# Kernel tuning notes

Measured on AMD Instinct MI355X. Metric: run time of the kernel, lower is better.

## Reference

```python
import jax, jax.numpy as jnp
import numpy as np

D_MODEL = 1024
NUM_HEADS = 16
D_K = D_MODEL // NUM_HEADS


def setup_inputs() -> dict:
    key = jax.random.key(0)
    ks = jax.random.split(key, 11)
    B, S = 2, 2048
    scale = 1.0 / np.sqrt(D_MODEL)
    inp = {
        "query": jax.random.normal(ks[0], (B, S, D_MODEL), jnp.float32),
        "key": jax.random.normal(ks[1], (B, S, D_MODEL), jnp.float32),
        "value": jax.random.normal(ks[2], (B, S, D_MODEL), jnp.float32),
        "Wq": jax.random.normal(ks[3], (D_MODEL, D_MODEL), jnp.float32) * scale,
        "bq": jnp.zeros((D_MODEL,), jnp.float32),
        "Wk": jax.random.normal(ks[4], (D_MODEL, D_MODEL), jnp.float32) * scale,
        "bk": jnp.zeros((D_MODEL,), jnp.float32),
        "Wv": jax.random.normal(ks[5], (D_MODEL, D_MODEL), jnp.float32) * scale,
        "bv": jnp.zeros((D_MODEL,), jnp.float32),
        "Wo": jax.random.normal(ks[6], (D_MODEL, D_MODEL), jnp.float32) * scale,
        "bo": jnp.zeros((D_MODEL,), jnp.float32),
    }
    return inp


def _split_heads(x):
    B, S, _ = x.shape
    return x.reshape(B, S, NUM_HEADS, D_K).transpose(0, 2, 1, 3)  # [B,H,S,d_k]


def reference(query, key, value, Wq, bq, Wk, bk, Wv, bv, Wo, bo):
    # Linear projections (torch Linear: x @ W.T + b)
    q = _split_heads(query @ Wq.T + bq)
    k = _split_heads(key @ Wk.T + bk)
    v = _split_heads(value @ Wv.T + bv)
    scores = jnp.einsum("bhqd,bhkd->bhqk", q, k) / jnp.sqrt(jnp.float32(D_K))
    probs = jax.nn.softmax(scores, axis=-1)
    out = jnp.einsum("bhqk,bhkd->bhqd", probs, v)  # [B,H,S,d_k]
    B, H, S, _ = out.shape
    out = out.transpose(0, 2, 1, 3).reshape(B, S, D_MODEL)
    return out @ Wo.T + bo
```

## Files before the change

kernel.cpp:

```cpp
#include <hip/hip_runtime.h>

#define D_MODEL 1024
#define NHEADS  16
#define DK      64
#define SEQ     2048
#define NBATCH  2
#define MTOT    (NBATCH * SEQ)

typedef _Float16 f16;
typedef _Float16 f16x4 __attribute__((ext_vector_type(4)));
typedef _Float16 f16x8 __attribute__((ext_vector_type(8)));
typedef float    f32x4 __attribute__((ext_vector_type(4)));
typedef float    f32x16 __attribute__((ext_vector_type(16)));

#define LOG2E 1.44269504088896340736f

__global__ __launch_bounds__(256) void cvt_f32_to_f16(
    const float* __restrict__ q, const float* __restrict__ k, const float* __restrict__ v,
    const float* __restrict__ wq, const float* __restrict__ wk,
    const float* __restrict__ wv, const float* __restrict__ wo,
    f16* __restrict__ qf, f16* __restrict__ kf, f16* __restrict__ vf,
    f16* __restrict__ wqh, f16* __restrict__ wkh, f16* __restrict__ wvh, f16* __restrict__ woh)
{
    const int z = blockIdx.y;
    const float* src; f16* dst; int n4;
    if (z == 0)      { src = q;  dst = qf;  n4 = MTOT * D_MODEL / 4; }
    else if (z == 1) { src = k;  dst = kf;  n4 = MTOT * D_MODEL / 4; }
    else if (z == 2) { src = v;  dst = vf;  n4 = MTOT * D_MODEL / 4; }
    else if (z == 3) { src = wq; dst = wqh; n4 = D_MODEL * D_MODEL / 4; }
    else if (z == 4) { src = wk; dst = wkh; n4 = D_MODEL * D_MODEL / 4; }
    else if (z == 5) { src = wv; dst = wvh; n4 = D_MODEL * D_MODEL / 4; }
    else             { src = wo; dst = woh; n4 = D_MODEL * D_MODEL / 4; }
    for (int i = blockIdx.x * 256 + threadIdx.x; i < n4; i += gridDim.x * 256) {
        float4 t = ((const float4*)src)[i];
        f16x4 o = {(f16)t.x, (f16)t.y, (f16)t.z, (f16)t.w};
        ((f16x4*)dst)[i] = o;
    }
}

__device__ __forceinline__ void gemm128_core(
    const f16* __restrict__ A, const f16* __restrict__ Wm,
    int m0, int n0, int kbeg, int kend, f32x16 (&acc)[2][2])
{
    __shared__ __align__(16) f16 As[4096];
    __shared__ __align__(16) f16 Bs[4096];

    const int t    = threadIdx.x;
    const int lane = t & 63;
    const int w    = t >> 6;
    const int l31  = lane & 31, kg = lane >> 5;
    const int wr   = w >> 1,    wc = w & 1;

    size_t offA[2], offB[2];
#pragma unroll
    for (int jj = 0; jj < 2; ++jj) {
        int s  = (w * 2 + jj) * 64 + lane;
        int ko = s >> 7, m = s & 127;
        offA[jj] = (size_t)(m0 + m) * D_MODEL + ko * 8;
        offB[jj] = (size_t)(n0 + m) * D_MODEL + ko * 8;
    }
    const int jb = __builtin_amdgcn_readfirstlane(w * 1024);

#pragma unroll
    for (int i = 0; i < 2; ++i)
#pragma unroll
        for (int j = 0; j < 2; ++j)
#pragma unroll
            for (int r = 0; r < 16; ++r) acc[i][j][r] = 0.f;

    auto* ldsA = (__attribute__((address_space(3))) f16*)As;
    auto* ldsB = (__attribute__((address_space(3))) f16*)Bs;

    for (int k0 = kbeg; k0 < kend; k0 += 32) {
#pragma unroll
        for (int jj = 0; jj < 2; ++jj) {
            __builtin_amdgcn_global_load_lds(
                (const __attribute__((address_space(1))) void*)(A + offA[jj] + k0),
                (__attribute__((address_space(3))) void*)(ldsA + jb + jj * 512),
                16, 0, 0);
            __builtin_amdgcn_global_load_lds(
                (const __attribute__((address_space(1))) void*)(Wm + offB[jj] + k0),
                (__attribute__((address_space(3))) void*)(ldsB + jb + jj * 512),
                16, 0, 0);
        }
        __syncthreads();

#pragma unroll
        for (int step = 0; step < 2; ++step) {
            const int ko = kg + 2 * step;
            f16x8 aF[2], bF[2];
#pragma unroll
            for (int ti = 0; ti < 2; ++ti) {
                aF[ti] = *(const f16x8*)&As[(ko * 128 + wr * 64 + ti * 32 + l31) * 8];
                bF[ti] = *(const f16x8*)&Bs[(ko * 128 + wc * 64 + ti * 32 + l31) * 8];
            }
#pragma unroll
            for (int ti = 0; ti < 2; ++ti)
#pragma unroll
                for (int tj = 0; tj < 2; ++tj)
                    acc[ti][tj] = __builtin_amdgcn_mfma_f32_32x32x16_f16(
                        aF[ti], bF[tj], acc[ti][tj], 0, 0, 0);
        }
        __syncthreads();
    }
}

__global__ __launch_bounds__(256, 3) void qkv_gemm(
    const f16* __restrict__ Qf, const f16* __restrict__ Kf, const f16* __restrict__ Vf,
    const f16* __restrict__ Wqh, const f16* __restrict__ Wkh, const f16* __restrict__ Wvh,
    const float* __restrict__ bq, const float* __restrict__ bk, const float* __restrict__ bv,
    f16* __restrict__ Qh, f16* __restrict__ Kh, f16* __restrict__ Vt)
{
    const int z = blockIdx.z;
    const f16*   A    = z == 0 ? Qf  : z == 1 ? Kf  : Vf;
    const f16*   Wm   = z == 0 ? Wqh : z == 1 ? Wkh : Wvh;
    const float* bias = z == 0 ? bq  : z == 1 ? bk  : bv;

    const int m0 = blockIdx.y * 128, n0 = blockIdx.x * 128;
    f32x16 acc[2][2];
    gemm128_core(A, Wm, m0, n0, 0, D_MODEL, acc);

    const int t = threadIdx.x, lane = t & 63, w = t >> 6;
    const int l31 = lane & 31, kg = lane >> 5;
    const int wr = w >> 1, wc = w & 1;

    if (z < 2) {
        f16* Out = z == 0 ? Qh : Kh;
        const float sc = z == 0 ? 0.125f * LOG2E : 1.0f;
#pragma unroll
        for (int tj = 0; tj < 2; ++tj) {
            const int col = n0 + wc * 64 + tj * 32 + l31;
            const float bc = bias[col];
#pragma unroll
            for (int ti = 0; ti < 2; ++ti)
#pragma unroll
                for (int r = 0; r < 16; ++r) {
                    const int row = m0 + wr * 64 + ti * 32 + (r & 3) + 8 * (r >> 2) + 4 * kg;
                    Out[(size_t)row * D_MODEL + col] = (f16)((acc[ti][tj][r] + bc) * sc);
                }
        }
    } else {
#pragma unroll
        for (int tj = 0; tj < 2; ++tj) {
            const int col = n0 + wc * 64 + tj * 32 + l31;
            const float bc = bias[col];
            const int h = col >> 6, d = col & 63;
#pragma unroll
            for (int ti = 0; ti < 2; ++ti)
#pragma unroll
                for (int r = 0; r < 16; ++r) {
                    const int row = m0 + wr * 64 + ti * 32 + (r & 3) + 8 * (r >> 2) + 4 * kg;
                    const int bb = row >> 11, s = row & (SEQ - 1);
                    Vt[(size_t)((bb * NHEADS + h) * DK + d) * SEQ + s] = (f16)(acc[ti][tj][r] + bc);
                }
        }
    }
}

__global__ __launch_bounds__(256, 3) void oproj_splitk(
    const f16* __restrict__ A, const f16* __restrict__ Wm,
    float* __restrict__ P0, float* __restrict__ P1)
{
    const int z = blockIdx.z;
    const int m0 = blockIdx.y * 128, n0 = blockIdx.x * 128;
    f32x16 acc[2][2];
    gemm128_core(A, Wm, m0, n0, z * 512, z * 512 + 512, acc);

    float* Out = z == 0 ? P0 : P1;
    const int t = threadIdx.x, lane = t & 63, w = t >> 6;
    const int l31 = lane & 31, kg = lane >> 5;
    const int wr = w >> 1, wc = w & 1;
#pragma unroll
    for (int tj = 0; tj < 2; ++tj) {
        const int col = n0 + wc * 64 + tj * 32 + l31;
#pragma unroll
        for (int ti = 0; ti < 2; ++ti)
#pragma unroll
            for (int r = 0; r < 16; ++r) {
                const int row = m0 + wr * 64 + ti * 32 + (r & 3) + 8 * (r >> 2) + 4 * kg;
                Out[(size_t)row * D_MODEL + col] = acc[ti][tj][r];
            }
    }
}

__global__ __launch_bounds__(256) void reduce_bias(
    const float* __restrict__ P0, const float* __restrict__ P1,
    const float* __restrict__ bias, float* __restrict__ Out)
{
    const int n4 = MTOT * D_MODEL / 4;
    for (int i = blockIdx.x * 256 + threadIdx.x; i < n4; i += gridDim.x * 256) {
        float4 a = ((const float4*)P0)[i];
        float4 b = ((const float4*)P1)[i];
        float4 c = ((const float4*)bias)[i & 255];
        float4 o = {a.x + b.x + c.x, a.y + b.y + c.y,
                    a.z + b.z + c.z, a.w + b.w + c.w};
        ((float4*)Out)[i] = o;
    }
}

__global__ __launch_bounds__(256, 4) void mha_mfma_v6(
    const f16* __restrict__ Qh, const f16* __restrict__ Kh,
    const f16* __restrict__ Vt, f16* __restrict__ Op, float* __restrict__ sp)
{
    __shared__ __align__(16) f16 Ks[4096];
    __shared__ __align__(16) f16 Vc[4096];
    __shared__ __align__(16) f16 Ps[128 * 68];

    const int t    = threadIdx.x;
    const int w    = t >> 6;
    const int lane = t & 63;
    const int quad = lane >> 4, l15 = lane & 15;

    const int qt = blockIdx.x, bh = blockIdx.y, half = blockIdx.z;
    const int b  = bh >> 4,    h  = bh & 15;
    const int q0 = qt * 128;

    f16x8 aQ[2][2];
#pragma unroll
    for (int s = 0; s < 2; ++s)
#pragma unroll
        for (int c = 0; c < 2; ++c)
            aQ[s][c] = *(const f16x8*)&Qh[
                (size_t)(b * SEQ + q0 + w * 32 + s * 16 + l15) * D_MODEL
                + h * DK + c * 32 + quad * 8];

    const f16* gK[2]; const f16* gV[2]; int ldst[2];
#pragma unroll
    for (int jj = 0; jj < 2; ++jj) {
        const int kc = w * 2 + jj;
        gK[jj] = Kh + (size_t)(b * SEQ + lane) * D_MODEL + h * DK + kc * 8;
        gV[jj] = Vt + (size_t)(bh * DK + lane) * SEQ + kc * 8;
        ldst[jj] = __builtin_amdgcn_readfirstlane(kc * 512);
    }
    auto* ldsK = (__attribute__((address_space(3))) f16*)Ks;
    auto* ldsV = (__attribute__((address_space(3))) f16*)Vc;

    const f16x8 onesB = {(f16)1.f, (f16)1.f, (f16)1.f, (f16)1.f,
                         (f16)1.f, (f16)1.f, (f16)1.f, (f16)1.f};

    f32x4 o[2][4];
#pragma unroll
    for (int s = 0; s < 2; ++s)
#pragma unroll
        for (int j = 0; j < 4; ++j) o[s][j] = (f32x4){0.f, 0.f, 0.f, 0.f};
    f32x4 sacc[2] = {(f32x4){0.f, 0.f, 0.f, 0.f}, (f32x4){0.f, 0.f, 0.f, 0.f}};

    const int kt0 = half * (SEQ / 128);
    for (int kt = kt0; kt < kt0 + SEQ / 128; ++kt) {
#pragma unroll
        for (int jj = 0; jj < 2; ++jj) {
            __builtin_amdgcn_global_load_lds(
                (const __attribute__((address_space(1))) void*)(gK[jj] + (size_t)kt * 64 * D_MODEL),
                (__attribute__((address_space(3))) void*)(ldsK + ldst[jj]), 16, 0, 0);
            __builtin_amdgcn_global_load_lds(
                (const __attribute__((address_space(1))) void*)(gV[jj] + kt * 64),
                (__attribute__((address_space(3))) void*)(ldsV + ldst[jj]), 16, 0, 0);
        }
        __syncthreads();

        f16x8 bK[4][2], bV[4][2];
#pragma unroll
        for (int f = 0; f < 4; ++f)
#pragma unroll
            for (int c = 0; c < 2; ++c) {
                const int slot = ((c * 4 + quad) * 64 + f * 16 + l15) * 8;
                bK[f][c] = *(const f16x8*)&Ks[slot];
                bV[f][c] = *(const f16x8*)&Vc[slot];
            }

#pragma unroll
        for (int s = 0; s < 2; ++s) {
            f32x4 sc[4];
#pragma unroll
            for (int f = 0; f < 4; ++f) {
                f32x4 a = (f32x4){0.f, 0.f, 0.f, 0.f};
                a = __builtin_amdgcn_mfma_f32_16x16x32_f16(aQ[s][0], bK[f][0], a, 0, 0, 0);
                a = __builtin_amdgcn_mfma_f32_16x16x32_f16(aQ[s][1], bK[f][1], a, 0, 0, 0);
                sc[f] = a;
            }

#pragma unroll
            for (int f = 0; f < 4; ++f)
#pragma unroll
                for (int r = 0; r < 4; ++r)
                    sc[f][r] = __builtin_exp2f(sc[f][r]);

#pragma unroll
            for (int f = 0; f < 4; ++f)
#pragma unroll
                for (int r = 0; r < 4; ++r)
                    Ps[(w * 32 + s * 16 + quad * 4 + r) * 68 + f * 16 + l15] = (f16)sc[f][r];

            f16x8 aP[2];
#pragma unroll
            for (int c = 0; c < 2; ++c) {
                const int off = (w * 32 + s * 16 + l15) * 68 + c * 32 + quad * 8;
                f16x4 lo = *(const f16x4*)&Ps[off];
                f16x4 hi = *(const f16x4*)&Ps[off + 4];
                aP[c] = __builtin_shufflevector(lo, hi, 0, 1, 2, 3, 4, 5, 6, 7);
            }

#pragma unroll
            for (int j = 0; j < 4; ++j) {
                o[s][j] = __builtin_amdgcn_mfma_f32_16x16x32_f16(aP[0], bV[j][0], o[s][j], 0, 0, 0);
                o[s][j] = __builtin_amdgcn_mfma_f32_16x16x32_f16(aP[1], bV[j][1], o[s][j], 0, 0, 0);
            }
            sacc[s] = __builtin_amdgcn_mfma_f32_16x16x32_f16(aP[0], onesB, sacc[s], 0, 0, 0);
            sacc[s] = __builtin_amdgcn_mfma_f32_16x16x32_f16(aP[1], onesB, sacc[s], 0, 0, 0);
        }
        __syncthreads();
    }

#pragma unroll
    for (int s = 0; s < 2; ++s)
#pragma unroll
        for (int r = 0; r < 4; ++r) {
            const int qrow = q0 + w * 32 + s * 16 + quad * 4 + r;
            const size_t base = ((size_t)(half * 32 + bh) * SEQ + qrow) * DK;
#pragma unroll
            for (int j = 0; j < 4; ++j)
                Op[base + j * 16 + l15] = (f16)o[s][j][r];
            if (l15 == 0)
                sp[(size_t)(half * 32 + bh) * SEQ + qrow] = sacc[s][r];
        }
}

__global__ __launch_bounds__(256) void mha_combine(
    const f16* __restrict__ Op, const float* __restrict__ sp,
    f16* __restrict__ ATh)
{
    const int gid = blockIdx.x * 256 + threadIdx.x;
    const int d4 = gid & 15;
    const int q  = (gid >> 4) & (SEQ - 1);
    const int bh = gid >> 15;
    const int b = bh >> 4, h = bh & 15;

    const size_t i0 = ((size_t)bh * SEQ + q) * DK + d4 * 4;
    const size_t i1 = ((size_t)(32 + bh) * SEQ + q) * DK + d4 * 4;
    f16x4 a = *(const f16x4*)&Op[i0];
    f16x4 c = *(const f16x4*)&Op[i1];
    const float inv = 1.f / (sp[(size_t)bh * SEQ + q] + sp[(size_t)(32 + bh) * SEQ + q]);
    f16x4 r;
#pragma unroll
    for (int m = 0; m < 4; ++m)
        r[m] = (f16)(((float)a[m] + (float)c[m]) * inv);
    *(f16x4*)&ATh[((size_t)(b * SEQ + q)) * D_MODEL + h * DK + d4 * 4] = r;
}

extern "C" void kernel_launch(void* const* d_in, const int* in_sizes, int n_in,
                              void* d_out, int out_size, void* d_ws, size_t ws_size,
                              hipStream_t stream)
{
    const float* query = (const float*)d_in[0];
    const float* key   = (const float*)d_in[1];
    const float* value = (const float*)d_in[2];
    const float* Wq    = (const float*)d_in[3];
    const float* bq    = (const float*)d_in[4];
    const float* Wk    = (const float*)d_in[5];
    const float* bk    = (const float*)d_in[6];
    const float* Wv    = (const float*)d_in[7];
    const float* bv    = (const float*)d_in[8];
    const float* Wo    = (const float*)d_in[9];
    const float* bo    = (const float*)d_in[10];
    float* out = (float*)d_out;

    f16* Qf  = (f16*)d_ws;
    f16* Kf  = Qf  + (size_t)MTOT * D_MODEL;
    f16* Vf  = Kf  + (size_t)MTOT * D_MODEL;
    f16* Wqh = Vf  + (size_t)MTOT * D_MODEL;
    f16* Wkh = Wqh + (size_t)D_MODEL * D_MODEL;
    f16* Wvh = Wkh + (size_t)D_MODEL * D_MODEL;
    f16* Woh = Wvh + (size_t)D_MODEL * D_MODEL;
    f16* Qh  = Woh + (size_t)D_MODEL * D_MODEL;
    f16* Kh  = Qh  + (size_t)MTOT * D_MODEL;
    f16* Vt  = Kh  + (size_t)MTOT * D_MODEL;
    f16* ATh = Vt  + (size_t)MTOT * D_MODEL;

    f16*   Op = Qf;
    float* sp = (float*)(Vf + (size_t)1024 * 1024);
    float* P0 = (float*)Qf;
    float* P1 = (float*)Qh;

    cvt_f32_to_f16<<<dim3(1024, 7), 256, 0, stream>>>(
        query, key, value, Wq, Wk, Wv, Wo, Qf, Kf, Vf, Wqh, Wkh, Wvh, Woh);

    qkv_gemm<<<dim3(D_MODEL / 128, MTOT / 128, 3), 256, 0, stream>>>(
        Qf, Kf, Vf, Wqh, Wkh, Wvh, bq, bk, bv, Qh, Kh, Vt);

    mha_mfma_v6<<<dim3(SEQ / 128, NBATCH * NHEADS, 2), 256, 0, stream>>>(
        Qh, Kh, Vt, Op, sp);

    mha_combine<<<dim3(MTOT * D_MODEL / 4 / 256), 256, 0, stream>>>(Op, sp, ATh);

    oproj_splitk<<<dim3(D_MODEL / 128, MTOT / 128, 2), 256, 0, stream>>>(ATh, Woh, P0, P1);

    reduce_bias<<<dim3(1024), 256, 0, stream>>>(P0, P1, bo, out);
}
```

Measured before the change: 267.2 us.

## Fuse fp32-to-fp16 activation conversion into QKV GEMM and reorder attention grid

The separate conversion pass over the query, key and value activations is removed. The QKV GEMM now loads fp32 A tiles into registers, converts them to fp16 and writes them to LDS itself, while weights still use direct global-to-LDS loads. This drops a full read/write pass over about 12M elements, at the cost of synchronous register-staged A loads inside the GEMM loop. The attention grid is also reordered so that batch-head is the fastest-varying block index, which changes how blocks of the same query tile share K/V in cache.

After: 268.9 us. Within noise of the previous version (+0.7%).

```diff
diff --git a/kernel.cpp b/kernel.cpp
--- a/kernel.cpp
+++ b/kernel.cpp
@@ -15,26 +15,136 @@
 
 #define LOG2E 1.44269504088896340736f
 
-__global__ __launch_bounds__(256) void cvt_f32_to_f16(
-    const float* __restrict__ q, const float* __restrict__ k, const float* __restrict__ v,
+__global__ __launch_bounds__(256) void cvt_w_f16(
     const float* __restrict__ wq, const float* __restrict__ wk,
     const float* __restrict__ wv, const float* __restrict__ wo,
-    f16* __restrict__ qf, f16* __restrict__ kf, f16* __restrict__ vf,
-    f16* __restrict__ wqh, f16* __restrict__ wkh, f16* __restrict__ wvh, f16* __restrict__ woh)
+    f16* __restrict__ wqh, f16* __restrict__ wkh,
+    f16* __restrict__ wvh, f16* __restrict__ woh)
 {
     const int z = blockIdx.y;
-    const float* src; f16* dst; int n4;
-    if (z == 0)      { src = q;  dst = qf;  n4 = MTOT * D_MODEL / 4; }
-    else if (z == 1) { src = k;  dst = kf;  n4 = MTOT * D_MODEL / 4; }
-    else if (z == 2) { src = v;  dst = vf;  n4 = MTOT * D_MODEL / 4; }
-    else if (z == 3) { src = wq; dst = wqh; n4 = D_MODEL * D_MODEL / 4; }
-    else if (z == 4) { src = wk; dst = wkh; n4 = D_MODEL * D_MODEL / 4; }
-    else if (z == 5) { src = wv; dst = wvh; n4 = D_MODEL * D_MODEL / 4; }
-    else             { src = wo; dst = woh; n4 = D_MODEL * D_MODEL / 4; }
+    const float* src = z == 0 ? wq : z == 1 ? wk : z == 2 ? wv : wo;
+    f16* dst        = z == 0 ? wqh : z == 1 ? wkh : z == 2 ? wvh : woh;
+    const int n4 = D_MODEL * D_MODEL / 4;
     for (int i = blockIdx.x * 256 + threadIdx.x; i < n4; i += gridDim.x * 256) {
         float4 t = ((const float4*)src)[i];
         f16x4 o = {(f16)t.x, (f16)t.y, (f16)t.z, (f16)t.w};
         ((f16x4*)dst)[i] = o;
+    }
+}
+
+__global__ __launch_bounds__(256, 3) void qkv_gemm(
+    const float* __restrict__ Q32, const float* __restrict__ K32, const float* __restrict__ V32,
+    const f16* __restrict__ Wqh, const f16* __restrict__ Wkh, const f16* __restrict__ Wvh,
+    const float* __restrict__ bq, const float* __restrict__ bk, const float* __restrict__ bv,
+    f16* __restrict__ Qh, f16* __restrict__ Kh, f16* __restrict__ Vt)
+{
+    __shared__ __align__(16) f16 As[4096];
+    __shared__ __align__(16) f16 Bs[4096];
+
+    const int z = blockIdx.z;
+    const float* A32  = z == 0 ? Q32 : z == 1 ? K32 : V32;
+    const f16*   Wm   = z == 0 ? Wqh : z == 1 ? Wkh : Wvh;
+    const float* bias = z == 0 ? bq  : z == 1 ? bk  : bv;
+
+    const int m0 = blockIdx.y * 128, n0 = blockIdx.x * 128;
+
+    const int t    = threadIdx.x;
+    const int lane = t & 63;
+    const int w    = t >> 6;
+    const int l31  = lane & 31, kg = lane >> 5;
+    const int wr   = w >> 1,    wc = w & 1;
+
+    const int ra = t >> 3;
+    const int kf = (t & 7) * 4;
+    const int ko = kf >> 3;
+    const int ki = kf & 7;
+    const float* Ap = &A32[(size_t)(m0 + ra) * D_MODEL + kf];
+
+    size_t offB[2];
+#pragma unroll
+    for (int jj = 0; jj < 2; ++jj) {
+        int s  = (w * 2 + jj) * 64 + lane;
+        int bko = s >> 7, bm = s & 127;
+        offB[jj] = (size_t)(n0 + bm) * D_MODEL + bko * 8;
+    }
+    const int jb = __builtin_amdgcn_readfirstlane(w * 1024);
+    auto* ldsB = (__attribute__((address_space(3))) f16*)Bs;
+
+    f32x16 acc[2][2];
+#pragma unroll
+    for (int i = 0; i < 2; ++i)
+#pragma unroll
+        for (int j = 0; j < 2; ++j)
+#pragma unroll
+            for (int r = 0; r < 16; ++r) acc[i][j][r] = 0.f;
+
+    for (int k0 = 0; k0 < D_MODEL; k0 += 32) {
+        float4 av[4];
+#pragma unroll
+        for (int r = 0; r < 4; ++r)
+            av[r] = *(const float4*)(Ap + (size_t)(32 * r) * D_MODEL + k0);
+#pragma unroll
+        for (int jj = 0; jj < 2; ++jj)
+            __builtin_amdgcn_global_load_lds(
+                (const __attribute__((address_space(1))) void*)(Wm + offB[jj] + k0),
+                (__attribute__((address_space(3))) void*)(ldsB + jb + jj * 512),
+                16, 0, 0);
+#pragma unroll
+        for (int r = 0; r < 4; ++r) {
+            f16x4 h = {(f16)av[r].x, (f16)av[r].y, (f16)av[r].z, (f16)av[r].w};
+            *(f16x4*)&As[(ko * 128 + ra + 32 * r) * 8 + ki] = h;
+        }
+        __syncthreads();
+
+#pragma unroll
+        for (int step = 0; step < 2; ++step) {
+            const int kk = kg + 2 * step;
+            f16x8 aF[2], bF[2];
+#pragma unroll
+            for (int ti = 0; ti < 2; ++ti) {
+                aF[ti] = *(const f16x8*)&As[(kk * 128 + wr * 64 + ti * 32 + l31) * 8];
+                bF[ti] = *(const f16x8*)&Bs[(kk * 128 + wc * 64 + ti * 32 + l31) * 8];
+            }
+#pragma unroll
+            for (int ti = 0; ti < 2; ++ti)
+#pragma unroll
+                for (int tj = 0; tj < 2; ++tj)
+                    acc[ti][tj] = __builtin_amdgcn_mfma_f32_32x32x16_f16(
+                        aF[ti], bF[tj], acc[ti][tj], 0, 0, 0);
+        }
+        __syncthreads();
+    }
+
+    if (z < 2) {
+        f16* Out = z == 0 ? Qh : Kh;
+        const float sc = z == 0 ? 0.125f * LOG2E : 1.0f;
+#pragma unroll
+        for (int tj = 0; tj < 2; ++tj) {
+            const int col = n0 + wc * 64 + tj * 32 + l31;
+            const float bc = bias[col];
+#pragma unroll
+            for (int ti = 0; ti < 2; ++ti)
+#pragma unroll
+                for (int r = 0; r < 16; ++r) {
+                    const int row = m0 + wr * 64 + ti * 32 + (r & 3) + 8 * (r >> 2) + 4 * kg;
+                    Out[(size_t)row * D_MODEL + col] = (f16)((acc[ti][tj][r] + bc) * sc);
+                }
+        }
+    } else {
+#pragma unroll
+        for (int tj = 0; tj < 2; ++tj) {
+            const int col = n0 + wc * 64 + tj * 32 + l31;
+            const float bc = bias[col];
+            const int h = col >> 6, d = col & 63;
+#pragma unroll
+            for (int ti = 0; ti < 2; ++ti)
+#pragma unroll
+                for (int r = 0; r < 16; ++r) {
+                    const int row = m0 + wr * 64 + ti * 32 + (r & 3) + 8 * (r >> 2) + 4 * kg;
+                    const int bb = row >> 11, s = row & (SEQ - 1);
+                    Vt[(size_t)((bb * NHEADS + h) * DK + d) * SEQ + s] = (f16)(acc[ti][tj][r] + bc);
+                }
+        }
     }
 }
 
@@ -87,12 +197,12 @@
 
 #pragma unroll
         for (int step = 0; step < 2; ++step) {
-            const int ko = kg + 2 * step;
+            const int kk = kg + 2 * step;
             f16x8 aF[2], bF[2];
 #pragma unroll
             for (int ti = 0; ti < 2; ++ti) {
-                aF[ti] = *(const f16x8*)&As[(ko * 128 + wr * 64 + ti * 32 + l31) * 8];
-                bF[ti] = *(const f16x8*)&Bs[(ko * 128 + wc * 64 + ti * 32 + l31) * 8];
+                aF[ti] = *(const f16x8*)&As[(kk * 128 + wr * 64 + ti * 32 + l31) * 8];
+                bF[ti] = *(const f16x8*)&Bs[(kk * 128 + wc * 64 + ti * 32 + l31) * 8];
             }
 #pragma unroll
             for (int ti = 0; ti < 2; ++ti)
@@ -102,58 +212,6 @@
                         aF[ti], bF[tj], acc[ti][tj], 0, 0, 0);
         }
         __syncthreads();
-    }
-}
-
-__global__ __launch_bounds__(256, 3) void qkv_gemm(
-    const f16* __restrict__ Qf, const f16* __restrict__ Kf, const f16* __restrict__ Vf,
-    const f16* __restrict__ Wqh, const f16* __restrict__ Wkh, const f16* __restrict__ Wvh,
-    const float* __restrict__ bq, const float* __restrict__ bk, const float* __restrict__ bv,
-    f16* __restrict__ Qh, f16* __restrict__ Kh, f16* __restrict__ Vt)
-{
-    const int z = blockIdx.z;
-    const f16*   A    = z == 0 ? Qf  : z == 1 ? Kf  : Vf;
-    const f16*   Wm   = z == 0 ? Wqh : z == 1 ? Wkh : Wvh;
-    const float* bias = z == 0 ? bq  : z == 1 ? bk  : bv;
-
-    const int m0 = blockIdx.y * 128, n0 = blockIdx.x * 128;
-    f32x16 acc[2][2];
-    gemm128_core(A, Wm, m0, n0, 0, D_MODEL, acc);
-
-    const int t = threadIdx.x, lane = t & 63, w = t >> 6;
-    const int l31 = lane & 31, kg = lane >> 5;
-    const int wr = w >> 1, wc = w & 1;
-
-    if (z < 2) {
-        f16* Out = z == 0 ? Qh : Kh;
-        const float sc = z == 0 ? 0.125f * LOG2E : 1.0f;
-#pragma unroll
-        for (int tj = 0; tj < 2; ++tj) {
-            const int col = n0 + wc * 64 + tj * 32 + l31;
-            const float bc = bias[col];
-#pragma unroll
-            for (int ti = 0; ti < 2; ++ti)
-#pragma unroll
-                for (int r = 0; r < 16; ++r) {
-                    const int row = m0 + wr * 64 + ti * 32 + (r & 3) + 8 * (r >> 2) + 4 * kg;
-                    Out[(size_t)row * D_MODEL + col] = (f16)((acc[ti][tj][r] + bc) * sc);
-                }
-        }
-    } else {
-#pragma unroll
-        for (int tj = 0; tj < 2; ++tj) {
-            const int col = n0 + wc * 64 + tj * 32 + l31;
-            const float bc = bias[col];
-            const int h = col >> 6, d = col & 63;
-#pragma unroll
-            for (int ti = 0; ti < 2; ++ti)
-#pragma unroll
-                for (int r = 0; r < 16; ++r) {
-                    const int row = m0 + wr * 64 + ti * 32 + (r & 3) + 8 * (r >> 2) + 4 * kg;
-                    const int bb = row >> 11, s = row & (SEQ - 1);
-                    Vt[(size_t)((bb * NHEADS + h) * DK + d) * SEQ + s] = (f16)(acc[ti][tj][r] + bc);
-                }
-        }
     }
 }
 
@@ -198,7 +256,7 @@
     }
 }
 
-__global__ __launch_bounds__(256, 4) void mha_mfma_v6(
+__global__ __launch_bounds__(256, 4) void mha_mfma_v7(
     const f16* __restrict__ Qh, const f16* __restrict__ Kh,
     const f16* __restrict__ Vt, f16* __restrict__ Op, float* __restrict__ sp)
 {
@@ -211,7 +269,7 @@
     const int lane = t & 63;
     const int quad = lane >> 4, l15 = lane & 15;
 
-    const int qt = blockIdx.x, bh = blockIdx.y, half = blockIdx.z;
+    const int bh = blockIdx.x, qt = blockIdx.y, half = blockIdx.z;
     const int b  = bh >> 4,    h  = bh & 15;
     const int q0 = qt * 128;
 
@@ -364,10 +422,8 @@
     const float* bo    = (const float*)d_in[10];
     float* out = (float*)d_out;
 
-    f16* Qf  = (f16*)d_ws;
-    f16* Kf  = Qf  + (size_t)MTOT * D_MODEL;
-    f16* Vf  = Kf  + (size_t)MTOT * D_MODEL;
-    f16* Wqh = Vf  + (size_t)MTOT * D_MODEL;
+    f16* S0  = (f16*)d_ws;
+    f16* Wqh = S0  + (size_t)12 * 1024 * 1024;
     f16* Wkh = Wqh + (size_t)D_MODEL * D_MODEL;
     f16* Wvh = Wkh + (size_t)D_MODEL * D_MODEL;
     f16* Woh = Wvh + (size_t)D_MODEL * D_MODEL;
@@ -376,18 +432,18 @@
     f16* Vt  = Kh  + (size_t)MTOT * D_MODEL;
     f16* ATh = Vt  + (size_t)MTOT * D_MODEL;
 
-    f16*   Op = Qf;
-    float* sp = (float*)(Vf + (size_t)1024 * 1024);
-    float* P0 = (float*)Qf;
+    f16*   Op = S0;
+    float* sp = (float*)(S0 + (size_t)9 * 1024 * 1024);
+    float* P0 = (float*)S0;
     float* P1 = (float*)Qh;
 
-    cvt_f32_to_f16<<<dim3(1024, 7), 256, 0, stream>>>(
-        query, key, value, Wq, Wk, Wv, Wo, Qf, Kf, Vf, Wqh, Wkh, Wvh, Woh);
+    cvt_w_f16<<<dim3(128, 4), 256, 0, stream>>>(
+        Wq, Wk, Wv, Wo, Wqh, Wkh, Wvh, Woh);
 
     qkv_gemm<<<dim3(D_MODEL / 128, MTOT / 128, 3), 256, 0, stream>>>(
-        Qf, Kf, Vf, Wqh, Wkh, Wvh, bq, bk, bv, Qh, Kh, Vt);
-
-    mha_mfma_v6<<<dim3(SEQ / 128, NBATCH * NHEADS, 2), 256, 0, stream>>>(
+        query, key, value, Wqh, Wkh, Wvh, bq, bk, bv, Qh, Kh, Vt);
+
+    mha_mfma_v7<<<dim3(NBATCH * NHEADS, SEQ / 128, 2), 256, 0, stream>>>(
         Qh, Kh, Vt, Op, sp);
 
     mha_combine<<<dim3(MTOT * D_MODEL / 4 / 256), 256, 0, stream>>>(Op, sp, ATh);
```
